# Performance work log

Hardware: AMD Instinct MI355X
Metric: run time of the kernel (lower is better)

Reference implementation:

```python
import jax, jax.numpy as jnp
import numpy as np

K = 20  # neighbors (includes self, as PyG knn(x,x,k) does)
B, P = 8, 2048


def _knn_idx(pts, k):
    # pts: [P, D] -> [P, k] indices of k nearest (self included, dist 0)
    sq = jnp.sum(pts * pts, axis=-1)
    dist = sq[:, None] + sq[None, :] - 2.0 * (pts @ pts.T)
    return jax.lax.top_k(-dist, k)[1]


def _edge_conv(x, W, b, k):
    # DynamicEdgeConv with single-Linear nn and max aggregation.
    # x: [B,P,D]; W: [C, 2D]; message = Lin([x_i, x_j - x_i])
    D = x.shape[-1]
    Wa, Wb = W[:, :D], W[:, D:]
    idx = jax.vmap(lambda p: _knn_idx(p, k))(x)                 # [B,P,k]
    nb = jax.vmap(lambda xb, ib: xb[ib])(x, idx)                # [B,P,k,D]
    msg = (x @ Wa.T)[:, :, None, :] + (nb - x[:, :, None, :]) @ Wb.T + b
    return jnp.max(msg, axis=2)                                 # [B,P,C]


def _lin(h, W, b):
    return h @ W.T + b


def setup_inputs() -> dict:
    key = jax.random.key(0)
    ks = jax.random.split(key, 16)
    N = B * P

    def w(k_, shape):
        fan_in = shape[-1]
        return (jax.random.normal(k_, shape, dtype=jnp.float32) / np.sqrt(fan_in)).astype(jnp.float32)

    inp = {
        "pos": jax.random.normal(ks[0], (N, 3), dtype=jnp.float32),
        "x": jax.random.normal(ks[1], (N, 3), dtype=jnp.float32),
        "features": jax.random.normal(ks[2], (N, 1344), dtype=jnp.float32),
        "batch": (jnp.arange(N) // P).astype(jnp.int64) if jax.config.jax_enable_x64 else (jnp.arange(N) // P).astype(jnp.int32),
        # filter_conv: Conv2d(1344,128,1) == Linear 1344->128
        "Wf": w(ks[3], (128, 1344)), "bf": jnp.zeros((128,), jnp.float32),
        # edge MLPs (single Linear each, plain_last)
        "W1": w(ks[4], (64, 2 * 134)), "b1": jnp.zeros((64,), jnp.float32),
        "W2": w(ks[5], (128, 2 * 64)), "b2": jnp.zeros((128,), jnp.float32),
        "W3": w(ks[6], (256, 2 * 128)), "b3": jnp.zeros((256,), jnp.float32),
        # fc1: Linear 576->1024
        "Wfc1": w(ks[7], (1024, 576)), "bfc1": jnp.zeros((1024,), jnp.float32),
        # fc2: 1024->512->256->23 with ReLU on hidden layers
        "Wfa": w(ks[8], (512, 1024)), "bfa": jnp.zeros((512,), jnp.float32),
        "Wfb": w(ks[9], (256, 512)), "bfb": jnp.zeros((256,), jnp.float32),
        "Wfc": w(ks[10], (23, 256)), "bfc": jnp.zeros((23,), jnp.float32),
    }
    return inp


def reference(pos, x, features, batch, Wf, bf, W1, b1, W2, b2, W3, b3,
              Wfc1, bfc1, Wfa, bfa, Wfb, bfb, Wfc, bfc):
    N = pos.shape[0]
    nB = int(batch[-1]) + 1
    nP = N // nB

    feats = _lin(features, Wf, bf)                              # [N,128] (1x1 conv)
    h0 = jnp.concatenate([pos, x, feats], axis=1).reshape(nB, nP, -1)  # [B,P,134]

    x1 = _edge_conv(h0, W1, b1, K)                              # [B,P,64]
    x2 = _edge_conv(x1, W2, b2, K)                              # [B,P,128]
    x3 = _edge_conv(x2, W3, b3, K)                              # [B,P,256]

    cat = jnp.concatenate([x1, x2, x3, feats.reshape(nB, nP, -1)], axis=-1)  # [B,P,576]
    h = _lin(cat, Wfc1, bfc1)                                   # [B,P,1024]
    g = jnp.max(h, axis=1)                                      # global_max_pool -> [B,1024]
    g = jax.nn.relu(_lin(g, Wfa, bfa))
    g = jax.nn.relu(_lin(g, Wfb, bfb))
    g = _lin(g, Wfc, bfc)
    return jax.nn.log_softmax(g, axis=1)                        # [B,23]
```

## Files before the change

### kernel.cpp

```cpp
#include <hip/hip_runtime.h>
#include <math.h>

#define PPB 2048
#define NBATCH 8
#define KNN 20

typedef __attribute__((ext_vector_type(8))) short short8;
typedef __attribute__((ext_vector_type(8))) __bf16 bf16x8;
typedef __attribute__((ext_vector_type(4))) float f32x4;

__global__ __launch_bounds__(256) void gemm_feats_kernel(
    const float* __restrict__ X, const float* __restrict__ W,
    float* __restrict__ fpart, int N) {
  const int KC = 336;
  int kc = blockIdx.z;
  const float* Xp = X + kc * KC;
  const float* Wp = W + kc * KC;
  float* Y = fpart + (size_t)kc * N * 128;
  __shared__ float Xs[8][132];
  __shared__ float Ws[8][132];
  int t = threadIdx.x;
  int tx = t & 15, ty = t >> 4;
  int i0 = blockIdx.y * 128;
  float acc[8][8];
#pragma unroll
  for (int r = 0; r < 8; ++r)
#pragma unroll
    for (int n = 0; n < 8; ++n) acc[r][n] = 0.f;

  for (int k0 = 0; k0 < KC; k0 += 8) {
#pragma unroll
    for (int p = 0; p < 4; ++p) {
      int e = t + p * 256, r = e >> 3, c = e & 7, k = k0 + c;
      Xs[c][r] = Xp[(size_t)(i0 + r) * 1344 + k];
      Ws[c][r] = Wp[(size_t)r * 1344 + k];
    }
    __syncthreads();
#pragma unroll
    for (int k = 0; k < 8; ++k) {
      float4 a0 = *(const float4*)&Xs[k][ty * 8];
      float4 a1 = *(const float4*)&Xs[k][ty * 8 + 4];
      float a[8] = {a0.x, a0.y, a0.z, a0.w, a1.x, a1.y, a1.z, a1.w};
      float4 b0 = *(const float4*)&Ws[k][tx * 8];
      float4 b1 = *(const float4*)&Ws[k][tx * 8 + 4];
      float bb[8] = {b0.x, b0.y, b0.z, b0.w, b1.x, b1.y, b1.z, b1.w};
#pragma unroll
      for (int r = 0; r < 8; ++r)
#pragma unroll
        for (int n = 0; n < 8; ++n) acc[r][n] += a[r] * bb[n];
    }
    __syncthreads();
  }
#pragma unroll
  for (int r = 0; r < 8; ++r) {
    size_t row = (size_t)(i0 + ty * 8 + r) * 128 + tx * 8;
#pragma unroll
    for (int n4 = 0; n4 < 2; ++n4) {
      float4 o;
      o.x = acc[r][n4 * 4 + 0]; o.y = acc[r][n4 * 4 + 1];
      o.z = acc[r][n4 * 4 + 2]; o.w = acc[r][n4 * 4 + 3];
      *(float4*)&Y[row + n4 * 4] = o;
    }
  }
}

__global__ __launch_bounds__(256) void reduce_feats_kernel(
    const float* __restrict__ fpart, const float* __restrict__ bias,
    float* __restrict__ catbuf, int N) {
  int e = blockIdx.x * 256 + threadIdx.x;
  size_t NP = (size_t)N * 128;
  int i = e >> 7, m = e & 127;
  float s = bias[m] + fpart[e] + fpart[NP + e] + fpart[2 * NP + e] + fpart[3 * NP + e];
  catbuf[(size_t)i * 576 + 448 + m] = s;
}

__global__ __launch_bounds__(256) void edge_gemm_kernel(
    const float* __restrict__ X, int ldx, int D,
    const float* __restrict__ W, int ldw, int M,
    float* __restrict__ A, float* __restrict__ Pb) {
  __shared__ float Xs[16][68];
  __shared__ float Ws[16][68];
  int t = threadIdx.x, tx = t & 15, ty = t >> 4;
  int nHalf = M >> 6;
  int mt = blockIdx.x;
  int is_b = (mt >= nHalf) ? 1 : 0;
  int m0 = (is_b ? mt - nHalf : mt) << 6;
  int koff = is_b ? D : 0;
  float* __restrict__ out = is_b ? Pb : A;
  int i0 = blockIdx.y * 64;
  float acc[4][4];
#pragma unroll
  for (int r = 0; r < 4; ++r)
#pragma unroll
    for (int n = 0; n < 4; ++n) acc[r][n] = 0.f;

  for (int k0 = 0; k0 < D; k0 += 16) {
#pragma unroll
    for (int p = 0; p < 4; ++p) {
      int e = t + p * 256, r = e >> 4, c = e & 15, k = k0 + c;
      Xs[c][r] = (k < D) ? X[(size_t)(i0 + r) * ldx + k] : 0.f;
      Ws[c][r] = (k < D) ? W[(size_t)(m0 + r) * ldw + koff + k] : 0.f;
    }
    __syncthreads();
#pragma unroll
    for (int kk = 0; kk < 16; ++kk) {
      float4 a4 = *(const float4*)&Xs[kk][ty * 4];
      float4 b4 = *(const float4*)&Ws[kk][tx * 4];
      float a[4] = {a4.x, a4.y, a4.z, a4.w};
      float bb[4] = {b4.x, b4.y, b4.z, b4.w};
#pragma unroll
      for (int r = 0; r < 4; ++r)
#pragma unroll
        for (int n = 0; n < 4; ++n) acc[r][n] += a[r] * bb[n];
    }
    __syncthreads();
  }
#pragma unroll
  for (int r = 0; r < 4; ++r) {
    float4 o;
    o.x = acc[r][0]; o.y = acc[r][1]; o.z = acc[r][2]; o.w = acc[r][3];
    *(float4*)&out[(size_t)(i0 + ty * 4 + r) * M + m0 + tx * 4] = o;
  }
}

__global__ __launch_bounds__(256) void cast_bf16_kernel(
    const float* __restrict__ src, unsigned short* __restrict__ dst, int n) {
  int e4 = (blockIdx.x * 256 + threadIdx.x) * 4;
  if (e4 >= n) return;
  float4 v = *(const float4*)&src[e4];
  ushort4 o;
  unsigned int u;
  u = __float_as_uint(v.x); o.x = (unsigned short)((u + 0x7fff + ((u >> 16) & 1)) >> 16);
  u = __float_as_uint(v.y); o.y = (unsigned short)((u + 0x7fff + ((u >> 16) & 1)) >> 16);
  u = __float_as_uint(v.z); o.z = (unsigned short)((u + 0x7fff + ((u >> 16) & 1)) >> 16);
  u = __float_as_uint(v.w); o.w = (unsigned short)((u + 0x7fff + ((u >> 16) & 1)) >> 16);
  *(ushort4*)&dst[e4] = o;
}

__global__ __launch_bounds__(256) void cast_hl_kernel(
    const float* __restrict__ X, int ldx, int D, int Kp,
    unsigned short* __restrict__ hi, unsigned short* __restrict__ lo) {
  int i = blockIdx.x;
  for (int k = threadIdx.x; k < Kp; k += 256) {
    float x = (k < D) ? X[(size_t)i * ldx + k] : 0.f;
    unsigned int u = __float_as_uint(x);
    unsigned short h = (unsigned short)((u + 0x7fff + ((u >> 16) & 1)) >> 16);
    float hf = __uint_as_float((unsigned int)h << 16);
    float r = x - hf;
    unsigned int v = __float_as_uint(r);
    unsigned short l16 = (unsigned short)((v + 0x7fff + ((v >> 16) & 1)) >> 16);
    hi[(size_t)i * Kp + k] = h;
    lo[(size_t)i * Kp + k] = l16;
  }
}

template <int KP>
__global__ __launch_bounds__(256) void dist_gemm2_kernel(
    const unsigned short* __restrict__ Xhi,
    const unsigned short* __restrict__ Xlo,
    const float* __restrict__ sq,
    float* __restrict__ dist, int zBase) {
  __shared__ unsigned short Ah[128][40];
  __shared__ unsigned short Al[128][40];
  __shared__ unsigned short Bh[64][40];
  __shared__ unsigned short Bl[64][40];
  int t = threadIdx.x;
  int l = t & 63, w = t >> 6;
  int z = blockIdx.z;
  size_t bbase = (size_t)(zBase + z) * PPB;
  int c0 = blockIdx.x * 64, q0 = blockIdx.y * 128;

  f32x4 acc[2][4];
#pragma unroll
  for (int qs = 0; qs < 2; ++qs)
#pragma unroll
    for (int cc = 0; cc < 4; ++cc) acc[qs][cc] = (f32x4){0.f, 0.f, 0.f, 0.f};

  for (int k0 = 0; k0 < KP; k0 += 32) {
    short8 sa[2][2];
#pragma unroll
    for (int p = 0; p < 2; ++p) {
      int e = t + p * 256, row = e >> 2, kg = e & 3;
      sa[p][0] = *(const short8*)&Xhi[(bbase + q0 + row) * KP + k0 + kg * 8];
      sa[p][1] = *(const short8*)&Xlo[(bbase + q0 + row) * KP + k0 + kg * 8];
    }
    int brow = t >> 2, bkg = t & 3;
    short8 sb0 = *(const short8*)&Xhi[(bbase + c0 + brow) * KP + k0 + bkg * 8];
    short8 sb1 = *(const short8*)&Xlo[(bbase + c0 + brow) * KP + k0 + bkg * 8];
    __syncthreads();
#pragma unroll
    for (int p = 0; p < 2; ++p) {
      int e = t + p * 256, row = e >> 2, kg = e & 3;
      *(short8*)&Ah[row][kg * 8] = sa[p][0];
      *(short8*)&Al[row][kg * 8] = sa[p][1];
    }
    *(short8*)&Bh[brow][bkg * 8] = sb0;
    *(short8*)&Bl[brow][bkg * 8] = sb1;
    __syncthreads();

    bf16x8 ah[2], al[2], bh[4], bl[4];
#pragma unroll
    for (int qs = 0; qs < 2; ++qs) {
      int row = w * 32 + qs * 16 + (l & 15);
      ah[qs] = __builtin_bit_cast(bf16x8, *(const short8*)&Ah[row][(l >> 4) * 8]);
      al[qs] = __builtin_bit_cast(bf16x8, *(const short8*)&Al[row][(l >> 4) * 8]);
    }
#pragma unroll
    for (int cc = 0; cc < 4; ++cc) {
      bh[cc] = __builtin_bit_cast(bf16x8, *(const short8*)&Bh[cc * 16 + (l & 15)][(l >> 4) * 8]);
      bl[cc] = __builtin_bit_cast(bf16x8, *(const short8*)&Bl[cc * 16 + (l & 15)][(l >> 4) * 8]);
    }
#pragma unroll
    for (int qs = 0; qs < 2; ++qs)
#pragma unroll
      for (int cc = 0; cc < 4; ++cc) {
        acc[qs][cc] = __builtin_amdgcn_mfma_f32_16x16x32_bf16(ah[qs], bh[cc], acc[qs][cc], 0, 0, 0);
        acc[qs][cc] = __builtin_amdgcn_mfma_f32_16x16x32_bf16(ah[qs], bl[cc], acc[qs][cc], 0, 0, 0);
        acc[qs][cc] = __builtin_amdgcn_mfma_f32_16x16x32_bf16(al[qs], bh[cc], acc[qs][cc], 0, 0, 0);
      }
  }
  float* dz = dist + (size_t)z * PPB * PPB;
#pragma unroll
  for (int cc = 0; cc < 4; ++cc) {
    int j = c0 + cc * 16 + (l & 15);
    float sqj = sq[bbase + j];
#pragma unroll
    for (int qs = 0; qs < 2; ++qs) {
      int qb = q0 + w * 32 + qs * 16 + (l >> 4) * 4;
#pragma unroll
      for (int r = 0; r < 4; ++r)
        dz[(size_t)(qb + r) * PPB + j] = sqj - 2.f * acc[qs][cc][r];
    }
  }
}

__global__ __launch_bounds__(256) void knn_sel3_kernel(
    const float* __restrict__ dist, int zBase, int* __restrict__ idx) {
  int z = blockIdx.y;
  int b = zBase + z;
  int q = blockIdx.x * 4 + (threadIdx.x >> 6);
  int lane = threadIdx.x & 63;
  const float* row = dist + ((size_t)z * PPB + q) * PPB + lane * 32;

  float v[32];
#pragma unroll
  for (int m4 = 0; m4 < 8; ++m4) {
    float4 f = *(const float4*)&row[m4 * 4];
    v[m4 * 4 + 0] = f.x; v[m4 * 4 + 1] = f.y;
    v[m4 * 4 + 2] = f.z; v[m4 * 4 + 3] = f.w;
  }
  float gv[8]; int gi[8];
#pragma unroll
  for (int g = 0; g < 8; ++g) {
    float bv = v[g * 4]; int bi = 0;
    if (v[g * 4 + 1] < bv) { bv = v[g * 4 + 1]; bi = 1; }
    if (v[g * 4 + 2] < bv) { bv = v[g * 4 + 2]; bi = 2; }
    if (v[g * 4 + 3] < bv) { bv = v[g * 4 + 3]; bi = 3; }
    gv[g] = bv; gi[g] = g * 4 + bi;
  }
  float lv = gv[0]; int lm = gi[0];
#pragma unroll
  for (int g = 1; g < 8; ++g)
    if (gv[g] < lv) { lv = gv[g]; lm = gi[g]; }
  unsigned u0 = __float_as_uint(lv);
  unsigned lk = u0 ^ (((int)u0 >> 31) | 0x80000000u);

  unsigned rm = 0;
#pragma unroll
  for (int s = 0; s < KNN; ++s) {
    unsigned bk = lk;
    int bj = lane * 32 + lm;
#pragma unroll
    for (int o = 1; o < 64; o <<= 1) {
      unsigned ok = __shfl_xor(bk, o);
      int oj = __shfl_xor(bj, o);
      if (ok < bk || (ok == bk && oj < bj)) { bk = ok; bj = oj; }
    }
    if (lane == 0)
      idx[((size_t)b * PPB + q) * KNN + s] = b * PPB + bj;
    if ((bj >> 5) == lane) {
      int m = bj & 31;
      rm |= (1u << m);
      int g = m >> 2;
      float e0 = v[0], e1 = v[1], e2 = v[2], e3 = v[3];
#pragma unroll
      for (int gg = 1; gg < 8; ++gg) {
        bool sel = (g == gg);
        e0 = sel ? v[gg * 4 + 0] : e0;
        e1 = sel ? v[gg * 4 + 1] : e1;
        e2 = sel ? v[gg * 4 + 2] : e2;
        e3 = sel ? v[gg * 4 + 3] : e3;
      }
      unsigned gm = (rm >> (g * 4)) & 15u;
      if (gm & 1u) e0 = 1e38f;
      if (gm & 2u) e1 = 1e38f;
      if (gm & 4u) e2 = 1e38f;
      if (gm & 8u) e3 = 1e38f;
      float nv = e0; int ni = 0;
      if (e1 < nv) { nv = e1; ni = 1; }
      if (e2 < nv) { nv = e2; ni = 2; }
      if (e3 < nv) { nv = e3; ni = 3; }
#pragma unroll
      for (int gg = 0; gg < 8; ++gg)
        if (g == gg) { gv[gg] = nv; gi[gg] = gg * 4 + ni; }
      lv = gv[0]; lm = gi[0];
#pragma unroll
      for (int gg = 1; gg < 8; ++gg)
        if (gv[gg] < lv) { lv = gv[gg]; lm = gi[gg]; }
      unsigned u = __float_as_uint(lv);
      lk = u ^ (((int)u >> 31) | 0x80000000u);
    }
  }
}

__global__ __launch_bounds__(256) void fc1max_mfma_kernel(
    const unsigned short* __restrict__ Xb, const unsigned short* __restrict__ Wb,
    const float* __restrict__ bias, float* __restrict__ partial) {
  __shared__ unsigned short Xs[64][40];
  __shared__ unsigned short Ws[64][40];
  __shared__ float red[4][64];
  int t = threadIdx.x;
  int l = t & 63, w = t >> 6;
  int b = blockIdx.z, pt = blockIdx.y;
  int i0 = b * PPB + pt * 64;
  int m0 = blockIdx.x * 64;
  int r_st = t >> 2;
  int c_st = (t & 3) * 8;

  f32x4 acc[4];
#pragma unroll
  for (int g = 0; g < 4; ++g) acc[g] = (f32x4){0.f, 0.f, 0.f, 0.f};

  for (int k0 = 0; k0 < 576; k0 += 32) {
    short8 xv = *(const short8*)&Xb[(size_t)(i0 + r_st) * 576 + k0 + c_st];
    short8 wv = *(const short8*)&Wb[(size_t)(m0 + r_st) * 576 + k0 + c_st];
    __syncthreads();
    *(short8*)&Xs[r_st][c_st] = xv;
    *(short8*)&Ws[r_st][c_st] = wv;
    __syncthreads();
    short8 ar = *(const short8*)&Xs[16 * w + (l & 15)][(l >> 4) * 8];
    bf16x8 av = __builtin_bit_cast(bf16x8, ar);
#pragma unroll
    for (int g = 0; g < 4; ++g) {
      short8 br = *(const short8*)&Ws[g * 16 + (l & 15)][(l >> 4) * 8];
      bf16x8 bv = __builtin_bit_cast(bf16x8, br);
      acc[g] = __builtin_amdgcn_mfma_f32_16x16x32_bf16(av, bv, acc[g], 0, 0, 0);
    }
  }
  float pm[4];
#pragma unroll
  for (int g = 0; g < 4; ++g) {
    float m = fmaxf(fmaxf(acc[g][0], acc[g][1]), fmaxf(acc[g][2], acc[g][3]));
    m = fmaxf(m, __shfl_xor(m, 16));
    m = fmaxf(m, __shfl_xor(m, 32));
    pm[g] = m;
  }
  if (l < 16) {
#pragma unroll
    for (int g = 0; g < 4; ++g) red[w][g * 16 + l] = pm[g];
  }
  __syncthreads();
  if (t < 64) {
    float mx = fmaxf(fmaxf(red[0][t], red[1][t]), fmaxf(red[2][t], red[3][t]));
    partial[((size_t)b * (PPB / 64) + pt) * 1024 + m0 + t] = mx + bias[m0 + t];
  }
}

__global__ __launch_bounds__(256) void gmax_kernel(
    const float* __restrict__ partial, float* __restrict__ g) {
  int b = blockIdx.y;
  int m = blockIdx.x * 256 + threadIdx.x;
  float mx = -INFINITY;
  for (int pt = 0; pt < PPB / 64; ++pt)
    mx = fmaxf(mx, partial[((size_t)b * (PPB / 64) + pt) * 1024 + m]);
  g[b * 1024 + m] = mx;
}

__global__ __launch_bounds__(192) void h0_kernel(
    const float* __restrict__ pos, const float* __restrict__ xin,
    const float* __restrict__ catbuf, float* __restrict__ h0) {
  int i = blockIdx.x;
  int d = threadIdx.x;
  if (d < 3)        h0[(size_t)i * 134 + d] = pos[i * 3 + d];
  else if (d < 6)   h0[(size_t)i * 134 + d] = xin[i * 3 + d - 3];
  else if (d < 134) h0[(size_t)i * 134 + d] = catbuf[(size_t)i * 576 + 448 + (d - 6)];
}

__global__ __launch_bounds__(64) void sq_kernel(
    const float* __restrict__ X, int ldx, int D, float* __restrict__ sq) {
  int i = blockIdx.x;
  int t = threadIdx.x;
  float s = 0.f;
  for (int k = t; k < D; k += 64) {
    float v = X[(size_t)i * ldx + k];
    s += v * v;
  }
  for (int off = 32; off > 0; off >>= 1) s += __shfl_down(s, off);
  if (t == 0) sq[i] = s;
}

__global__ __launch_bounds__(256) void edge_out_kernel(
    const float* __restrict__ A, const float* __restrict__ Pb, int M,
    const float* __restrict__ bias, const int* __restrict__ idx,
    float* __restrict__ Y, int ldy) {
  int i = blockIdx.x;
  int t = threadIdx.x;
  __shared__ int nbs[KNN];
  if (t < KNN) nbs[t] = idx[(size_t)i * KNN + t];
  __syncthreads();
  for (int m = t; m < M; m += 256) {
    float mx = -INFINITY;
#pragma unroll
    for (int kk = 0; kk < KNN; ++kk)
      mx = fmaxf(mx, Pb[(size_t)nbs[kk] * M + m]);
    Y[(size_t)i * ldy + m] = A[(size_t)i * M + m] + bias[m] - Pb[(size_t)i * M + m] + mx;
  }
}

__global__ __launch_bounds__(256) void mlp2_kernel(
    const float* __restrict__ X, const float* __restrict__ W,
    const float* __restrict__ bias, float* __restrict__ Y,
    int D, int M, int do_relu) {
  int b = blockIdx.y;
  int m = blockIdx.x * 4 + (threadIdx.x >> 6);
  int lane = threadIdx.x & 63;
  const float* xr = X + (size_t)b * D;
  const float* wr = W + (size_t)m * D;
  float s = 0.f;
  for (int k = lane * 4; k < D; k += 256) {
    float4 xv = *(const float4*)&xr[k];
    float4 wv = *(const float4*)&wr[k];
    s += xv.x * wv.x + xv.y * wv.y + xv.z * wv.z + xv.w * wv.w;
  }
#pragma unroll
  for (int o = 32; o > 0; o >>= 1) s += __shfl_down(s, o);
  if (lane == 0) {
    s += bias[m];
    if (do_relu) s = fmaxf(s, 0.f);
    Y[(size_t)b * M + m] = s;
  }
}

__global__ __launch_bounds__(256) void final2_kernel(
    const float* __restrict__ X, const float* __restrict__ W,
    const float* __restrict__ bias, float* __restrict__ out) {
  int b = blockIdx.x;
  int w = threadIdx.x >> 6, lane = threadIdx.x & 63;
  __shared__ float lg[23];
  const float* xr = X + (size_t)b * 256;
  float4 xv = *(const float4*)&xr[lane * 4];
  for (int c = w; c < 23; c += 4) {
    const float* wr = W + (size_t)c * 256;
    float4 wv = *(const float4*)&wr[lane * 4];
    float s = xv.x * wv.x + xv.y * wv.y + xv.z * wv.z + xv.w * wv.w;
#pragma unroll
    for (int o = 32; o > 0; o >>= 1) s += __shfl_down(s, o);
    if (lane == 0) lg[c] = s + bias[c];
  }
  __syncthreads();
  if (threadIdx.x == 0) {
    float mx = lg[0];
    for (int c = 1; c < 23; ++c) mx = fmaxf(mx, lg[c]);
    float s = 0.f;
    for (int c = 0; c < 23; ++c) s += expf(lg[c] - mx);
    float lse = mx + logf(s);
    for (int c = 0; c < 23; ++c) out[b * 23 + c] = lg[c] - lse;
  }
}


extern "C" void kernel_launch(void* const* d_in, const int* in_sizes, int n_in,
                              void* d_out, int out_size, void* d_ws, size_t ws_size,
                              hipStream_t stream) {
  const float* pos      = (const float*)d_in[0];
  const float* xin      = (const float*)d_in[1];
  const float* features = (const float*)d_in[2];
  const float* Wf   = (const float*)d_in[4];
  const float* bf   = (const float*)d_in[5];
  const float* W1   = (const float*)d_in[6];
  const float* b1   = (const float*)d_in[7];
  const float* W2   = (const float*)d_in[8];
  const float* b2   = (const float*)d_in[9];
  const float* W3   = (const float*)d_in[10];
  const float* b3   = (const float*)d_in[11];
  const float* Wfc1 = (const float*)d_in[12];
  const float* bfc1 = (const float*)d_in[13];
  const float* Wfa  = (const float*)d_in[14];
  const float* bfa  = (const float*)d_in[15];
  const float* Wfb  = (const float*)d_in[16];
  const float* bfb  = (const float*)d_in[17];
  const float* Wfc  = (const float*)d_in[18];
  const float* bfc  = (const float*)d_in[19];
  float* out = (float*)d_out;

  const int N = in_sizes[0] / 3;

  char* base = (char*)d_ws;
  size_t off = 0;
  auto alloc = [&](size_t bytes) {
    void* p = base + off;
    off += (bytes + 255) & ~(size_t)255;
    return p;
  };
  float* catbuf  = (float*)alloc((size_t)N * 576 * 4);
  float* h0      = (float*)alloc((size_t)N * 134 * 4);
  float* Abuf    = (float*)alloc((size_t)N * 256 * 4);
  float* Pbbuf   = (float*)alloc((size_t)N * 256 * 4);
  unsigned short* Xhi = (unsigned short*)alloc((size_t)N * 160 * 2);
  unsigned short* Xlo = (unsigned short*)alloc((size_t)N * 160 * 2);
  float* sqbuf   = (float*)alloc((size_t)N * 4);
  int*   idxbuf  = (int*)  alloc((size_t)N * KNN * 4);
  float* partial = (float*)alloc((size_t)NBATCH * (PPB / 64) * 1024 * 4);
  float* g       = (float*)alloc((size_t)NBATCH * 1024 * 4);
  float* ga      = (float*)alloc((size_t)NBATCH * 512 * 4);
  float* gb      = (float*)alloc((size_t)NBATCH * 256 * 4);

  const size_t distBatch = (size_t)PPB * PPB * 4;
  int nz;
  float* dist;
  if (ws_size >= off + 8 * distBatch + 256) {
    nz = 8;  dist = (float*)alloc(8 * distBatch);
  } else if (ws_size >= off + 4 * distBatch + 256) {
    nz = 4;  dist = (float*)alloc(4 * distBatch);
  } else {
    nz = 2;  dist = Abuf;
  }

  float* fpart = Abuf;
  unsigned short* catb16 = (unsigned short*)Abuf;
  unsigned short* Wb16   = (unsigned short*)h0;

  gemm_feats_kernel<<<dim3(1, N / 128, 4), 256, 0, stream>>>(features, Wf, fpart, N);
  reduce_feats_kernel<<<(N * 128) / 256, 256, 0, stream>>>(fpart, bf, catbuf, N);

  h0_kernel<<<N, 192, 0, stream>>>(pos, xin, catbuf, h0);

  struct Layer {
    const float* Xin; int ldx; int D; int Kp;
    const float* W; int ldw;
    const float* bias; int M;
    float* Yout;
  };
  Layer L[3] = {
      {h0,          134, 134, 160, W1, 268, b1,  64, catbuf + 0},
      {catbuf + 0,  576,  64,  64, W2, 128, b2, 128, catbuf + 64},
      {catbuf + 64, 576, 128, 128, W3, 256, b3, 256, catbuf + 192},
  };

  for (int l = 0; l < 3; ++l) {
    sq_kernel<<<N, 64, 0, stream>>>(L[l].Xin, L[l].ldx, L[l].D, sqbuf);
    cast_hl_kernel<<<N, 256, 0, stream>>>(L[l].Xin, L[l].ldx, L[l].D, L[l].Kp, Xhi, Xlo);
    for (int p = 0; p < NBATCH; p += nz) {
      if (L[l].Kp == 160)
        dist_gemm2_kernel<160><<<dim3(PPB / 64, PPB / 128, nz), 256, 0, stream>>>(
            Xhi, Xlo, sqbuf, dist, p);
      else if (L[l].Kp == 64)
        dist_gemm2_kernel<64><<<dim3(PPB / 64, PPB / 128, nz), 256, 0, stream>>>(
            Xhi, Xlo, sqbuf, dist, p);
      else
        dist_gemm2_kernel<128><<<dim3(PPB / 64, PPB / 128, nz), 256, 0, stream>>>(
            Xhi, Xlo, sqbuf, dist, p);
      knn_sel3_kernel<<<dim3(PPB / 4, nz), 256, 0, stream>>>(dist, p, idxbuf);
    }
    edge_gemm_kernel<<<dim3((2 * L[l].M) / 64, N / 64), 256, 0, stream>>>(
        L[l].Xin, L[l].ldx, L[l].D, L[l].W, L[l].ldw, L[l].M, Abuf, Pbbuf);
    edge_out_kernel<<<N, 256, 0, stream>>>(
        Abuf, Pbbuf, L[l].M, L[l].bias, idxbuf, L[l].Yout, 576);
  }

  cast_bf16_kernel<<<(N * 576) / 1024, 256, 0, stream>>>(catbuf, catb16, N * 576);
  cast_bf16_kernel<<<(1024 * 576) / 1024, 256, 0, stream>>>(Wfc1, Wb16, 1024 * 576);

  fc1max_mfma_kernel<<<dim3(1024 / 64, PPB / 64, NBATCH), 256, 0, stream>>>(
      catb16, Wb16, bfc1, partial);
  gmax_kernel<<<dim3(1024 / 256, NBATCH), 256, 0, stream>>>(partial, g);

  mlp2_kernel<<<dim3(512 / 4, NBATCH), 256, 0, stream>>>(g,  Wfa, bfa, ga, 1024, 512, 1);
  mlp2_kernel<<<dim3(256 / 4, NBATCH), 256, 0, stream>>>(ga, Wfb, bfb, gb, 512, 256, 1);
  final2_kernel<<<NBATCH, 256, 0, stream>>>(gb, Wfc, bfc, out);
}
```

Before: 688.9 us.

## Compute feature projection with split-bf16 MFMA and fuse row norms into cast

Replaces the fp32 SIMT feature GEMM (1344->128) with a path that splits features and weights into bf16 hi/lo parts and multiplies them with three MFMA ops per tile, writing bias-added results straight into the concat buffer. This path runs only when the workspace is large enough to hold the split copies. The cast kernel now also computes each row's squared norm with a shared-memory reduction, which removes the separate sq kernel per layer. The extra cast passes over the 1344-wide features add memory traffic, and the hi/lo split gives slightly lower precision than fp32.

```diff
diff --git a/kernel.cpp b/kernel.cpp
--- a/kernel.cpp
+++ b/kernel.cpp
@@ -72,6 +72,56 @@
   int i = e >> 7, m = e & 127;
   float s = bias[m] + fpart[e] + fpart[NP + e] + fpart[2 * NP + e] + fpart[3 * NP + e];
   catbuf[(size_t)i * 576 + 448 + m] = s;
+}
+
+__global__ __launch_bounds__(256) void feats_mfma_kernel(
+    const unsigned short* __restrict__ Xh, const unsigned short* __restrict__ Xl,
+    const unsigned short* __restrict__ Wh, const unsigned short* __restrict__ Wl,
+    const float* __restrict__ bias, float* __restrict__ catbuf) {
+  __shared__ unsigned short XsH[64][40], XsL[64][40];
+  __shared__ unsigned short WsH[64][40], WsL[64][40];
+  int t = threadIdx.x;
+  int l = t & 63, w = t >> 6;
+  int i0 = blockIdx.y * 64, m0 = blockIdx.x * 64;
+  int r_st = t >> 2, c_st = (t & 3) * 8;
+
+  f32x4 acc[4];
+#pragma unroll
+  for (int g = 0; g < 4; ++g) acc[g] = (f32x4){0.f, 0.f, 0.f, 0.f};
+
+  for (int k0 = 0; k0 < 1344; k0 += 32) {
+    short8 xh = *(const short8*)&Xh[(size_t)(i0 + r_st) * 1344 + k0 + c_st];
+    short8 xl = *(const short8*)&Xl[(size_t)(i0 + r_st) * 1344 + k0 + c_st];
+    short8 wh = *(const short8*)&Wh[(size_t)(m0 + r_st) * 1344 + k0 + c_st];
+    short8 wl = *(const short8*)&Wl[(size_t)(m0 + r_st) * 1344 + k0 + c_st];
+    __syncthreads();
+    *(short8*)&XsH[r_st][c_st] = xh;
+    *(short8*)&XsL[r_st][c_st] = xl;
+    *(short8*)&WsH[r_st][c_st] = wh;
+    *(short8*)&WsL[r_st][c_st] = wl;
+    __syncthreads();
+    bf16x8 ah = __builtin_bit_cast(bf16x8, *(const short8*)&XsH[16 * w + (l & 15)][(l >> 4) * 8]);
+    bf16x8 al = __builtin_bit_cast(bf16x8, *(const short8*)&XsL[16 * w + (l & 15)][(l >> 4) * 8]);
+#pragma unroll
+    for (int g = 0; g < 4; ++g) {
+      bf16x8 bh = __builtin_bit_cast(bf16x8, *(const short8*)&WsH[g * 16 + (l & 15)][(l >> 4) * 8]);
+      bf16x8 bl = __builtin_bit_cast(bf16x8, *(const short8*)&WsL[g * 16 + (l & 15)][(l >> 4) * 8]);
+      acc[g] = __builtin_amdgcn_mfma_f32_16x16x32_bf16(ah, bh, acc[g], 0, 0, 0);
+      acc[g] = __builtin_amdgcn_mfma_f32_16x16x32_bf16(ah, bl, acc[g], 0, 0, 0);
+      acc[g] = __builtin_amdgcn_mfma_f32_16x16x32_bf16(al, bh, acc[g], 0, 0, 0);
+    }
+  }
+  int qr = (l >> 4) * 4;
+#pragma unroll
+  for (int g = 0; g < 4; ++g) {
+    int col = m0 + g * 16 + (l & 15);
+    float bv = bias[col];
+#pragma unroll
+    for (int r = 0; r < 4; ++r) {
+      int row = i0 + w * 16 + qr + r;
+      catbuf[(size_t)row * 576 + 448 + col] = acc[g][r] + bv;
+    }
+  }
 }
 
 __global__ __launch_bounds__(256) void edge_gemm_kernel(
@@ -139,9 +189,13 @@
 
 __global__ __launch_bounds__(256) void cast_hl_kernel(
     const float* __restrict__ X, int ldx, int D, int Kp,
-    unsigned short* __restrict__ hi, unsigned short* __restrict__ lo) {
+    unsigned short* __restrict__ hi, unsigned short* __restrict__ lo,
+    float* __restrict__ sq) {
+  __shared__ float red[256];
   int i = blockIdx.x;
-  for (int k = threadIdx.x; k < Kp; k += 256) {
+  int t = threadIdx.x;
+  float s = 0.f;
+  for (int k = t; k < Kp; k += 256) {
     float x = (k < D) ? X[(size_t)i * ldx + k] : 0.f;
     unsigned int u = __float_as_uint(x);
     unsigned short h = (unsigned short)((u + 0x7fff + ((u >> 16) & 1)) >> 16);
@@ -151,7 +205,15 @@
     unsigned short l16 = (unsigned short)((v + 0x7fff + ((v >> 16) & 1)) >> 16);
     hi[(size_t)i * Kp + k] = h;
     lo[(size_t)i * Kp + k] = l16;
-  }
+    s += x * x;
+  }
+  red[t] = s;
+  __syncthreads();
+  for (int off = 128; off > 0; off >>= 1) {
+    if (t < off) red[t] += red[t + off];
+    __syncthreads();
+  }
+  if (t == 0) sq[i] = red[0];
 }
 
 template <int KP>
@@ -384,19 +446,6 @@
   if (d < 3)        h0[(size_t)i * 134 + d] = pos[i * 3 + d];
   else if (d < 6)   h0[(size_t)i * 134 + d] = xin[i * 3 + d - 3];
   else if (d < 134) h0[(size_t)i * 134 + d] = catbuf[(size_t)i * 576 + 448 + (d - 6)];
-}
-
-__global__ __launch_bounds__(64) void sq_kernel(
-    const float* __restrict__ X, int ldx, int D, float* __restrict__ sq) {
-  int i = blockIdx.x;
-  int t = threadIdx.x;
-  float s = 0.f;
-  for (int k = t; k < D; k += 64) {
-    float v = X[(size_t)i * ldx + k];
-    s += v * v;
-  }
-  for (int off = 32; off > 0; off >>= 1) s += __shfl_down(s, off);
-  if (t == 0) sq[i] = s;
 }
 
 __global__ __launch_bounds__(256) void edge_out_kernel(
@@ -530,8 +579,21 @@
   unsigned short* catb16 = (unsigned short*)Abuf;
   unsigned short* Wb16   = (unsigned short*)h0;
 
-  gemm_feats_kernel<<<dim3(1, N / 128, 4), 256, 0, stream>>>(features, Wf, fpart, N);
-  reduce_feats_kernel<<<(N * 128) / 256, 256, 0, stream>>>(fpart, bf, catbuf, N);
+  if (nz == 8) {
+    unsigned short* featHi = (unsigned short*)dist;
+    unsigned short* featLo = featHi + (size_t)N * 1344;
+    unsigned short* WfHi   = (unsigned short*)partial;
+    unsigned short* WfLo   = WfHi + (size_t)128 * 1344;
+    cast_hl_kernel<<<N, 256, 0, stream>>>(features, 1344, 1344, 1344,
+                                          featHi, featLo, sqbuf);
+    cast_hl_kernel<<<128, 256, 0, stream>>>(Wf, 1344, 1344, 1344,
+                                            WfHi, WfLo, sqbuf);
+    feats_mfma_kernel<<<dim3(2, N / 64), 256, 0, stream>>>(
+        featHi, featLo, WfHi, WfLo, bf, catbuf);
+  } else {
+    gemm_feats_kernel<<<dim3(1, N / 128, 4), 256, 0, stream>>>(features, Wf, fpart, N);
+    reduce_feats_kernel<<<(N * 128) / 256, 256, 0, stream>>>(fpart, bf, catbuf, N);
+  }
 
   h0_kernel<<<N, 192, 0, stream>>>(pos, xin, catbuf, h0);
 
@@ -548,8 +610,8 @@
   };
 
   for (int l = 0; l < 3; ++l) {
-    sq_kernel<<<N, 64, 0, stream>>>(L[l].Xin, L[l].ldx, L[l].D, sqbuf);
-    cast_hl_kernel<<<N, 256, 0, stream>>>(L[l].Xin, L[l].ldx, L[l].D, L[l].Kp, Xhi, Xlo);
+    cast_hl_kernel<<<N, 256, 0, stream>>>(L[l].Xin, L[l].ldx, L[l].D, L[l].Kp,
+                                          Xhi, Xlo, sqbuf);
     for (int p = 0; p < NBATCH; p += nz) {
       if (L[l].Kp == 160)
         dist_gemm2_kernel<160><<<dim3(PPB / 64, PPB / 128, nz), 256, 0, stream>>>(
```

Result: no change. 693.8 us (+0.7%).
